# Performance work log

Hardware: AMD Instinct MI355X
Metric: run time of the kernel (lower is better)

Reference implementation:

```python
import jax, jax.numpy as jnp
import numpy as np
from itertools import combinations

N_COLS = 16   # number of input features (columns of xl/xu)
ADD = 3       # max subset order
ALPHA = 0.5   # primary compare weight
BETA = 0.8    # tie-break compare weight
BATCH = 65536


def _bitmask(combo):
    m = 0
    for i in combo:
        m |= 1 << i
    return m


def _build_plan(n, add):
    """Static DP plan: for each subset length, gather indices of combo[1:] (left)
    and combo[:-1] (right) among previously computed columns; plus final bitmask order."""
    items = list(range(n))
    index_dict = {(i,): i for i in items}
    count = n
    plan = []
    for length in range(2, min(add, n) + 1):
        combos = list(combinations(items, length))
        if not combos:
            continue
        left = np.array([index_dict[c[1:]] for c in combos], dtype=np.int32)
        right = np.array([index_dict[c[:-1]] for c in combos], dtype=np.int32)
        for c in combos:
            index_dict[c] = count
            count += 1
        plan.append((left, right))
    order = np.array([index_dict[c] for c in sorted(index_dict, key=_bitmask)], dtype=np.int32)
    return plan, order

_PLAN, _ORDER = _build_plan(N_COLS, ADD)


def setup_inputs() -> dict:
    key = jax.random.key(0)
    k1, k2 = jax.random.split(key)
    a = jax.random.uniform(k1, (BATCH, N_COLS), dtype=jnp.float32)
    b = jax.random.uniform(k2, (BATCH, N_COLS), dtype=jnp.float32)
    # valid intervals: xl <= xu elementwise
    xl = jnp.minimum(a, b)
    xu = jnp.maximum(a, b)
    return {"xl": xl, "xu": xu}


def _select_pair(ll, lu, rl, ru):
    # alpha-weighted score; pick the interval with SMALLER score (choose_right when cur > nxt)
    cur = (1.0 - ALPHA) * ll + ALPHA * lu
    nxt = (1.0 - ALPHA) * rl + ALPHA * ru
    # tie-break with beta-weighted score
    beta_cur = (1.0 - BETA) * ll + BETA * lu
    beta_nxt = (1.0 - BETA) * rl + BETA * ru
    choose_right = jnp.where(cur == nxt, beta_cur > beta_nxt, cur > nxt)
    res_l = jnp.where(choose_right, rl, ll)
    res_u = jnp.where(choose_right, ru, lu)
    return res_l, res_u


def reference(xl, xu):
    # mat_* grow by one block per subset length; gathers use static index arrays
    mat_l, mat_u = xl, xu
    for left_idx, right_idx in _PLAN:
        ll = mat_l[:, left_idx]
        lu = mat_u[:, left_idx]
        rl = mat_l[:, right_idx]
        ru = mat_u[:, right_idx]
        res_l, res_u = _select_pair(ll, lu, rl, ru)
        mat_l = jnp.concatenate([mat_l, res_l], axis=1)
        mat_u = jnp.concatenate([mat_u, res_u], axis=1)
    # reorder columns by subset bitmask, as in _reorder_by_bitmask
    return mat_l[:, _ORDER], mat_u[:, _ORDER]
```

## Files before the change

kernel.cpp:

```cpp
#include <hip/hip_runtime.h>
#include <cstdint>

#define NCOLS  696
#define NGROUP 174
#define NREC   136
#define RPB    4
#define BLOCK  256

typedef float v4f __attribute__((ext_vector_type(4)));

constexpr int pr(int a, int b) { return 16 + b * (b - 1) / 2 + a; }

struct alignas(8) RecSrc { uint16_t d[NREC]; };
constexpr RecSrc make_recs() {
    RecSrc t{};
    for (int a = 0; a < 16; ++a) t.d[a] = (uint16_t)(a | (a << 8));
    int p = 16;
    for (int b = 1; b < 16; ++b)
        for (int a = 0; a < b; ++a)
            t.d[p++] = (uint16_t)(a | (b << 8));
    return t;
}

struct alignas(8) ColTbl { uint16_t d[NCOLS]; };
constexpr ColTbl make_cols() {
    ColTbl t{};
    int p = 0;
    for (int h = 0; h < 16; ++h) {
        t.d[p++] = (uint16_t)(h | (h << 8));
        for (int j = 0; j < h; ++j) {
            int pjh = pr(j, h);
            t.d[p++] = (uint16_t)(pjh | (pjh << 8));
            for (int i = 0; i < j; ++i)
                t.d[p++] = (uint16_t)(pr(j, h) | (pr(i, j) << 8));
        }
    }
    return t;
}

__constant__ RecSrc g_recs = make_recs();
__constant__ ColTbl g_cols = make_cols();

__device__ __forceinline__ float2 selpair(float2 L, float2 R) {
    float curL = __fadd_rn(L.x, L.y);
    float curR = __fadd_rn(R.x, R.y);
    float bL = __fadd_rn(__fmul_rn(0.2f, L.x), __fmul_rn(0.8f, L.y));
    float bR = __fadd_rn(__fmul_rn(0.2f, R.x), __fmul_rn(0.8f, R.y));
    bool choose_right = (curL == curR) ? (bL > bR) : (curL > curR);
    return choose_right ? R : L;
}

__device__ __forceinline__ float2 col_compute(const float2* __restrict__ rec,
                                              uint32_t d) {
    float2 L = rec[d & 255u];
    float2 R = rec[(d >> 8) & 255u];
    return selpair(L, R);
}

__global__ __launch_bounds__(BLOCK, 8) void minint_kernel(
    const float* __restrict__ xl, const float* __restrict__ xu,
    float* __restrict__ out, int batch)
{
    __shared__ float2 vals[RPB][16];
    __shared__ float2 recs[RPB][NREC];
    const int t    = threadIdx.x;
    const int w    = t >> 6;
    const int lane = t & 63;
    const int row  = blockIdx.x * RPB + w;

    if (lane < 16) {
        vals[w][lane] = make_float2(xl[row * 16 + lane], xu[row * 16 + lane]);
    }
    __builtin_amdgcn_wave_barrier();

    const float2* v = vals[w];

    for (int r = lane; r < NREC; r += 64) {
        uint32_t s = g_recs.d[r];
        float2 lo = v[s & 15u];
        float2 hi = v[(s >> 8) & 15u];
        recs[w][r] = selpair(hi, lo);
    }
    __builtin_amdgcn_wave_barrier();

    const int rowg = row;
    const float2* rec = recs[w];
    float* outl = out + (size_t)rowg * NCOLS;
    float* outu = out + (size_t)batch * NCOLS + (size_t)rowg * NCOLS;
    const ushort4* cols = (const ushort4*)g_cols.d;

    for (int g = lane; g < NGROUP; g += 64) {
        ushort4 d4 = cols[g];
        float2 c0 = col_compute(rec, d4.x);
        float2 c1 = col_compute(rec, d4.y);
        float2 c2 = col_compute(rec, d4.z);
        float2 c3 = col_compute(rec, d4.w);
        v4f rl = { c0.x, c1.x, c2.x, c3.x };
        v4f ru = { c0.y, c1.y, c2.y, c3.y };
        *(v4f*)(outl + 4 * g) = rl;
        *(v4f*)(outu + 4 * g) = ru;
    }
}

extern "C" void kernel_launch(void* const* d_in, const int* in_sizes, int n_in,
                              void* d_out, int out_size, void* d_ws, size_t ws_size,
                              hipStream_t stream) {
    const float* xl = (const float*)d_in[0];
    const float* xu = (const float*)d_in[1];
    float* out = (float*)d_out;
    const int batch = in_sizes[0] / 16;
    const int grid  = batch / RPB;
    minint_kernel<<<grid, BLOCK, 0, stream>>>(xl, xu, out, batch);
}
```

Before: 385.0 us.

## Map one row per lane and recompute pair intervals inline

Each wave now handles one row per lane, split across two waves by column range, instead of one wave cooperating on a single row. The 136-entry intermediate pair table in shared memory is gone: each column recomputes its pair selection from the 16 staged inputs and carries the last pair result in a register. This removes the intra-wave barriers and per-row table staging. In exchange, every lane writes 32-byte chunks to a different row, so global stores are no longer coalesced across the wave, and the kernel does extra selection arithmetic per column.

```diff
diff --git a/kernel.cpp b/kernel.cpp
--- a/kernel.cpp
+++ b/kernel.cpp
@@ -1,45 +1,29 @@
 #include <hip/hip_runtime.h>
 #include <cstdint>
 
-#define NCOLS  696
-#define NGROUP 174
-#define NREC   136
-#define RPB    4
-#define BLOCK  256
+#define NCOLS   696
+#define RG      64
+#define BLOCK   256
+#define SPLIT   344
+#define VSTRIDE 17
 
 typedef float v4f __attribute__((ext_vector_type(4)));
 
-constexpr int pr(int a, int b) { return 16 + b * (b - 1) / 2 + a; }
-
-struct alignas(8) RecSrc { uint16_t d[NREC]; };
-constexpr RecSrc make_recs() {
-    RecSrc t{};
-    for (int a = 0; a < 16; ++a) t.d[a] = (uint16_t)(a | (a << 8));
-    int p = 16;
-    for (int b = 1; b < 16; ++b)
-        for (int a = 0; a < b; ++a)
-            t.d[p++] = (uint16_t)(a | (b << 8));
-    return t;
-}
-
-struct alignas(8) ColTbl { uint16_t d[NCOLS]; };
-constexpr ColTbl make_cols() {
-    ColTbl t{};
+struct alignas(16) Tab { uint32_t d[NCOLS]; };
+constexpr Tab make_tab() {
+    Tab t{};
     int p = 0;
     for (int h = 0; h < 16; ++h) {
-        t.d[p++] = (uint16_t)(h | (h << 8));
+        t.d[p++] = (uint32_t)(h | (h << 4));
         for (int j = 0; j < h; ++j) {
-            int pjh = pr(j, h);
-            t.d[p++] = (uint16_t)(pjh | (pjh << 8));
+            t.d[p++] = (uint32_t)(j | (h << 4));
             for (int i = 0; i < j; ++i)
-                t.d[p++] = (uint16_t)(pr(j, h) | (pr(i, j) << 8));
+                t.d[p++] = (uint32_t)(i | (j << 4) | 256u);
         }
     }
     return t;
 }
-
-__constant__ RecSrc g_recs = make_recs();
-__constant__ ColTbl g_cols = make_cols();
+__constant__ Tab g_tab = make_tab();
 
 __device__ __forceinline__ float2 selpair(float2 L, float2 R) {
     float curL = __fadd_rn(L.x, L.y);
@@ -50,55 +34,67 @@
     return choose_right ? R : L;
 }
 
-__device__ __forceinline__ float2 col_compute(const float2* __restrict__ rec,
-                                              uint32_t d) {
-    float2 L = rec[d & 255u];
-    float2 R = rec[(d >> 8) & 255u];
-    return selpair(L, R);
-}
-
-__global__ __launch_bounds__(BLOCK, 8) void minint_kernel(
+__global__ __launch_bounds__(BLOCK, 2) void minint_kernel(
     const float* __restrict__ xl, const float* __restrict__ xu,
     float* __restrict__ out, int batch)
 {
-    __shared__ float2 vals[RPB][16];
-    __shared__ float2 recs[RPB][NREC];
+    __shared__ float2 vv[4][RG * VSTRIDE];
     const int t    = threadIdx.x;
     const int w    = t >> 6;
     const int lane = t & 63;
-    const int row  = blockIdx.x * RPB + w;
+    const int rg   = blockIdx.x * 2 + (w >> 1);
+    const int row  = rg * RG + lane;
+    const int half = w & 1;
 
-    if (lane < 16) {
-        vals[w][lane] = make_float2(xl[row * 16 + lane], xu[row * 16 + lane]);
+    const float4* l4 = (const float4*)(xl + (size_t)row * 16);
+    const float4* u4 = (const float4*)(xu + (size_t)row * 16);
+    float2* vrow = &vv[w][lane * VSTRIDE];
+#pragma unroll
+    for (int q = 0; q < 4; ++q) {
+        float4 a = l4[q], b = u4[q];
+        vrow[4 * q + 0] = make_float2(a.x, b.x);
+        vrow[4 * q + 1] = make_float2(a.y, b.y);
+        vrow[4 * q + 2] = make_float2(a.z, b.z);
+        vrow[4 * q + 3] = make_float2(a.w, b.w);
     }
-    __builtin_amdgcn_wave_barrier();
 
-    const float2* v = vals[w];
+    const int p0  = half ? SPLIT : 0;
+    const int nch = (half ? (NCOLS - SPLIT) : SPLIT) / 8;
+    const uint4* tabs = (const uint4*)g_tab.d;
 
-    for (int r = lane; r < NREC; r += 64) {
-        uint32_t s = g_recs.d[r];
-        float2 lo = v[s & 15u];
-        float2 hi = v[(s >> 8) & 15u];
-        recs[w][r] = selpair(hi, lo);
-    }
-    __builtin_amdgcn_wave_barrier();
+    float* rl = out + (size_t)row * NCOLS + p0;
+    float* ru = rl + (size_t)batch * NCOLS;
 
-    const int rowg = row;
-    const float2* rec = recs[w];
-    float* outl = out + (size_t)rowg * NCOLS;
-    float* outu = out + (size_t)batch * NCOLS + (size_t)rowg * NCOLS;
-    const ushort4* cols = (const ushort4*)g_cols.d;
+    float2 Lc = make_float2(0.0f, 0.0f);
 
-    for (int g = lane; g < NGROUP; g += 64) {
-        ushort4 d4 = cols[g];
-        float2 c0 = col_compute(rec, d4.x);
-        float2 c1 = col_compute(rec, d4.y);
-        float2 c2 = col_compute(rec, d4.z);
-        float2 c3 = col_compute(rec, d4.w);
-        v4f rl = { c0.x, c1.x, c2.x, c3.x };
-        v4f ru = { c0.y, c1.y, c2.y, c3.y };
-        *(v4f*)(outl + 4 * g) = rl;
-        *(v4f*)(outu + 4 * g) = ru;
+    for (int k = 0; k < nch; ++k) {
+        const uint4 ta = tabs[(p0 >> 2) + 2 * k];
+        const uint4 tb = tabs[(p0 >> 2) + 2 * k + 1];
+        const uint32_t ds[8] = {ta.x, ta.y, ta.z, ta.w, tb.x, tb.y, tb.z, tb.w};
+        float cl[8], cu[8];
+#pragma unroll
+        for (int s = 0; s < 8; ++s) {
+            const uint32_t d = ds[s];
+            float2 Vx = vrow[d & 15u];
+            float2 Vy = vrow[(d >> 4) & 15u];
+            float2 T1 = selpair(Vy, Vx);
+            float2 o;
+            if (d & 256u) {
+                o = selpair(Lc, T1);
+            } else {
+                Lc = T1;
+                o  = T1;
+            }
+            cl[s] = o.x; cu[s] = o.y;
+        }
+        v4f a0 = {cl[0], cl[1], cl[2], cl[3]};
+        v4f a1 = {cl[4], cl[5], cl[6], cl[7]};
+        v4f b0 = {cu[0], cu[1], cu[2], cu[3]};
+        v4f b1 = {cu[4], cu[5], cu[6], cu[7]};
+        *(v4f*)(rl + 8 * k)     = a0;
+        *(v4f*)(rl + 8 * k + 4) = a1;
+        *(v4f*)(ru + 8 * k)     = b0;
+        *(v4f*)(ru + 8 * k + 4) = b1;
     }
 }
 
@@ -109,6 +105,6 @@
     const float* xu = (const float*)d_in[1];
     float* out = (float*)d_out;
     const int batch = in_sizes[0] / 16;
-    const int grid  = batch / RPB;
+    const int grid  = batch / (2 * RG);
     minint_kernel<<<grid, BLOCK, 0, stream>>>(xl, xu, out, batch);
 }
```

Result: slower. 628.4 us (+63.2%).
